# Performance work log

Measured on AMD Instinct MI355X. Metric: run time of the kernel, lower is better.

The kernel has to match this reference:

```python
import jax, jax.numpy as jnp
import numpy as np

PAD = 0.1
RESO = 128           # plane_resolution
HID = 128            # hidden_dim
CDIM = 128           # c_dim
NBLK = 5             # n_blocks
PLANES = (('xz', (0, 2)), ('xy', (0, 1)), ('yz', (1, 2)))


def normalize_coordinate(p, dims):
    # p: (B,T,3) -> (B,T,2) in [0, 1)
    xy = p[..., list(dims)] / (1.0 + PAD + 1e-3) + 0.5
    return jnp.clip(xy, 0.0, 1.0 - 1e-5)


def coordinate2index(xy, reso):
    g = (xy * reso).astype(jnp.int32)          # (B,T,2)
    return g[..., 0] + reso * g[..., 1]        # (B,T) flat cell index


def scatter_max_gather(vals, idx, n_cells):
    # vals: (B,T,F), idx: (B,T) -> per-cell max gathered back to points (B,T,F)
    B, T, F = vals.shape
    flat_idx = (idx + jnp.arange(B, dtype=idx.dtype)[:, None] * n_cells).reshape(-1)
    fea = jax.ops.segment_max(vals.reshape(B * T, F), flat_idx, num_segments=B * n_cells)
    return fea[flat_idx].reshape(B, T, F)


def scatter_mean_plane(c, idx, n_cells):
    # c: (B,T,C), idx: (B,T) -> (B, n_cells, C); empty cells stay 0
    B, T, C = c.shape
    flat_idx = (idx + jnp.arange(B, dtype=idx.dtype)[:, None] * n_cells).reshape(-1)
    s = jax.ops.segment_sum(c.reshape(B * T, C), flat_idx, num_segments=B * n_cells)
    cnt = jax.ops.segment_sum(jnp.ones((B * T,), c.dtype), flat_idx, num_segments=B * n_cells)
    return (s / jnp.maximum(cnt, 1.0)[:, None]).reshape(B, n_cells, C)


def resnet_block(x, W0, b0, W1, b1, Ws):
    # ResnetBlockFC(2H -> H), size_h = H, shortcut = Linear(no bias)
    net = jax.nn.relu(x) @ W0 + b0
    dx = jax.nn.relu(net) @ W1 + b1
    return x @ Ws + dx


def setup_inputs() -> dict:
    key = jax.random.key(0)
    ks = jax.random.split(key, 10)
    B, T = 2, 32768
    s = 0.05
    return {
        'p': jax.random.uniform(ks[0], (B, T, 3), jnp.float32, -0.5, 0.5),
        'fc_pos_W': s * jax.random.normal(ks[1], (3, 2 * HID), jnp.float32),
        'fc_pos_b': s * jax.random.normal(ks[2], (2 * HID,), jnp.float32),
        'blocks_W0': s * jax.random.normal(ks[3], (NBLK, 2 * HID, HID), jnp.float32),
        'blocks_b0': s * jax.random.normal(ks[4], (NBLK, HID), jnp.float32),
        'blocks_W1': s * jax.random.normal(ks[5], (NBLK, HID, HID), jnp.float32),
        'blocks_b1': s * jax.random.normal(ks[6], (NBLK, HID), jnp.float32),
        'blocks_Ws': s * jax.random.normal(ks[7], (NBLK, 2 * HID, HID), jnp.float32),
        'fc_c_W': s * jax.random.normal(ks[8], (HID, CDIM), jnp.float32),
        'fc_c_b': s * jax.random.normal(ks[9], (CDIM,), jnp.float32),
    }


def reference(p, fc_pos_W, fc_pos_b, blocks_W0, blocks_b0, blocks_W1, blocks_b1,
              blocks_Ws, fc_c_W, fc_c_b):
    B, T, _ = p.shape
    R2 = RESO * RESO
    index = {k: coordinate2index(normalize_coordinate(p, d), RESO) for k, d in PLANES}

    net = p @ fc_pos_W + fc_pos_b                       # (B,T,2H)
    net = resnet_block(net, blocks_W0[0], blocks_b0[0],
                       blocks_W1[0], blocks_b1[0], blocks_Ws[0])  # (B,T,H)
    for i in range(1, NBLK):
        pooled = sum(scatter_max_gather(net, index[k], R2) for k, _ in PLANES)
        net = jnp.concatenate([net, pooled], axis=-1)   # (B,T,2H)
        net = resnet_block(net, blocks_W0[i], blocks_b0[i],
                           blocks_W1[i], blocks_b1[i], blocks_Ws[i])

    c = net @ fc_c_W + fc_c_b                           # (B,T,C)
    planes = []
    for k, _ in PLANES:  # order: xz, xy, yz
        fea = scatter_mean_plane(c, index[k], R2)       # (B,R2,C)
        planes.append(fea.transpose(0, 2, 1).reshape(B, CDIM, RESO, RESO))
    return jnp.stack(planes)                            # (3,B,C,R,R)
```

## Files before the change

kernel.cpp:

```cpp
#include <hip/hip_runtime.h>

#define TT 65536
#define R2 16384

typedef _Float16 f16x8 __attribute__((ext_vector_type(8)));
typedef float    f32x4 __attribute__((ext_vector_type(4)));
typedef unsigned u32x4 __attribute__((ext_vector_type(4)));

#define MFMA16 __builtin_amdgcn_mfma_f32_16x16x32_f16

__device__ __forceinline__ unsigned short f2h(float f){
    _Float16 h = (_Float16)f;
    return __builtin_bit_cast(unsigned short, h);
}
__device__ __forceinline__ float h2f(unsigned short u){
    return (float)__builtin_bit_cast(_Float16, u);
}
__device__ __forceinline__ unsigned relu2(unsigned w){
    unsigned s = w & 0x80008000u;
    unsigned mask = ((s >> 15) * 0x7FFFu) | s;
    return w & ~mask;
}
__device__ __forceinline__ float nrm(float a){
    float v = a / 1.101f + 0.5f;
    v = fmaxf(v, 0.0f);
    v = fminf(v, 0.99999f);
    return v;
}

__global__ __launch_bounds__(256) void k_repack(const float* __restrict__ W0,
        const float* __restrict__ W1, const float* __restrict__ Ws,
        const float* __restrict__ Wc, unsigned short* __restrict__ out,
        int* __restrict__ cnt){
    __shared__ unsigned short lh[4096];
    int b = blockIdx.x, tid = threadIdx.x;

    int gid = b*256 + tid;
    if (gid < 24576){ u32x4 z = {0,0,0,0}; ((u32x4*)cnt)[gid] = z; }

    const float* src; int obase;
    if (b < 100){
        int i = b/20, rr = b%20;
        if (rr < 8){       src = W0 + (size_t)i*32768 + rr*4096;      obase = i*81920 + rr*4096; }
        else if (rr < 12){ int ks=rr-8;  src = W1 + (size_t)i*16384 + ks*4096; obase = i*81920 + 32768 + ks*4096; }
        else {             int ks=rr-12; src = Ws + (size_t)i*32768 + ks*4096; obase = i*81920 + 49152 + ks*4096; }
    } else { int ks = b-100; src = Wc + ks*4096; obase = 409600 + ks*4096; }

    #pragma unroll
    for (int m = 0; m < 16; m++){
        int gi = m*256 + tid;
        lh[gi] = f2h(src[gi]);
    }
    __syncthreads();

    #pragma unroll
    for (int g2 = 0; g2 < 2; g2++){
        int base = tid*16 + g2*8;
        int l = (base >> 3) & 63, t = (base >> 9) & 7;
        int n = t*16 + (l & 15), kb = (l >> 4)*8;
        unsigned short h[8];
        #pragma unroll
        for (int j = 0; j < 8; j++) h[j] = lh[(kb + j)*128 + n];
        u32x4 pk;
        #pragma unroll
        for (int q = 0; q < 4; q++)
            pk[q] = (unsigned)h[2*q] | ((unsigned)h[2*q+1] << 16);
        *(u32x4*)(&out[obase + base]) = pk;
    }
}

__global__ __launch_bounds__(256) void k_idxhist(const float* __restrict__ p,
        int* __restrict__ idx, int* __restrict__ cnt){
    int pt = blockIdx.x*256 + threadIdx.x;
    float p0 = p[pt*3+0], p1 = p[pt*3+1], p2 = p[pt*3+2];
    int g0 = (int)(nrm(p0)*128.f);
    int g1 = (int)(nrm(p1)*128.f);
    int g2 = (int)(nrm(p2)*128.f);
    int i0 = g0 + 128*g2, i1 = g0 + 128*g1, i2 = g1 + 128*g2;
    idx[0*TT + pt] = i0;
    idx[1*TT + pt] = i1;
    idx[2*TT + pt] = i2;
    int b14 = (pt >> 15) << 14;
    atomicAdd(&cnt[0*32768 + b14 + i0], 1);
    atomicAdd(&cnt[1*32768 + b14 + i1], 1);
    atomicAdd(&cnt[2*32768 + b14 + i2], 1);
}

__global__ __launch_bounds__(1024) void k_scan(const int* cnt,
        int* __restrict__ cs, int* cp){
    __shared__ int wsum[16];
    int pl = blockIdx.x, tid = threadIdx.x;
    int lane = tid & 63, wid = tid >> 6;
    const int* c = cnt + pl*32768;
    int v[32], tot = 0;
    #pragma unroll
    for (int j = 0; j < 32; j++){ v[j] = c[tid*32 + j]; tot += v[j]; }
    int x = tot;
    #pragma unroll
    for (int off = 1; off < 64; off <<= 1){
        int y = __shfl_up(x, off, 64);
        if (lane >= off) x += y;
    }
    if (lane == 63) wsum[wid] = x;
    __syncthreads();
    int woff = 0;
    #pragma unroll
    for (int j = 0; j < 16; j++) woff += (j < wid) ? wsum[j] : 0;
    int run = woff + x - tot;
    #pragma unroll
    for (int j = 0; j < 32; j++){
        cs[pl*32769 + tid*32 + j] = run;
        cp[pl*32768 + tid*32 + j] = run;
        run += v[j];
    }
    if (tid == 1023) cs[pl*32769 + 32768] = TT;
}

__global__ __launch_bounds__(256) void k_scatter(const int* __restrict__ idx,
        int* __restrict__ cp, int* __restrict__ srt){
    int pt = blockIdx.x*256 + threadIdx.x;
    int b14 = (pt >> 15) << 14;
    #pragma unroll
    for (int pl = 0; pl < 3; pl++){
        int pos = atomicAdd(&cp[pl*32768 + b14 + idx[pl*TT + pt]], 1);
        srt[pl*TT + pos] = pt;
    }
}

__global__ __launch_bounds__(256) void k_pool3(const unsigned short* __restrict__ xb,
        const int* __restrict__ srt, const int* __restrict__ cs,
        unsigned short* __restrict__ mxp){
    int pl = blockIdx.y;
    const int* srtp = srt + (size_t)pl*TT;
    const int* csp  = cs  + (size_t)pl*32769;
    int lane = threadIdx.x & 63, w = threadIdx.x >> 6;
    int g = lane >> 4, l16 = lane & 15;
    int cbase = (blockIdx.x*4 + w)*4;
    for (int c = cbase; c < cbase + 4; c++){
        int s = csp[c], e = csp[c+1];
        if (s == e) continue;
        float fm[8];
        #pragma unroll
        for (int j = 0; j < 8; j++) fm[j] = -1e30f;
        for (int i = s + g; i < e; i += 4){
            int pt = srtp[i];
            u32x4 v = *(const u32x4*)(xb + (size_t)pt*128 + l16*8);
            #pragma unroll
            for (int q = 0; q < 4; q++){
                unsigned u = v[q];
                fm[2*q]   = fmaxf(fm[2*q],   h2f((unsigned short)(u & 0xFFFF)));
                fm[2*q+1] = fmaxf(fm[2*q+1], h2f((unsigned short)(u >> 16)));
            }
        }
        #pragma unroll
        for (int j = 0; j < 8; j++){
            fm[j] = fmaxf(fm[j], __shfl_xor(fm[j], 16, 64));
            fm[j] = fmaxf(fm[j], __shfl_xor(fm[j], 32, 64));
        }
        if (g == 0){
            u32x4 pk;
            #pragma unroll
            for (int q = 0; q < 4; q++)
                pk[q] = (unsigned)f2h(fm[2*q]) | ((unsigned)f2h(fm[2*q+1]) << 16);
            ((u32x4*)(mxp + ((size_t)pl*32768 + c)*128))[l16] = pk;
        }
    }
}

__global__ __launch_bounds__(256, 2) void k_resnet(
        const unsigned short* __restrict__ xin,
        unsigned short* __restrict__ xout,
        const unsigned short* __restrict__ wp,
        const float* __restrict__ b0, const float* __restrict__ b1,
        const int* __restrict__ idx, const unsigned short* __restrict__ mxp,
        const float* __restrict__ pin, const float* __restrict__ fW,
        const float* __restrict__ fb,
        const unsigned short* __restrict__ wc, const float* __restrict__ bc){
    __shared__ __align__(16) unsigned short lds[36864];
    unsigned short* lw0 = lds;
    unsigned short* lw1 = lds + 16384;
    unsigned short* lt  = lds + 32768;
    int tid = threadIdx.x, w = tid >> 6, lane = tid & 63;
    int quad = lane >> 4, l15 = lane & 15;
    int m0 = blockIdx.x*128 + w*32;
    float b0v[8], b1v[8];
    #pragma unroll
    for (int t = 0; t < 8; t++){ b0v[t] = b0[t*16 + l15]; b1v[t] = b1[t*16 + l15]; }

    u32x4 pre[8];
    auto preload = [&](const unsigned short* src){
        const u32x4* g = (const u32x4*)src;
        #pragma unroll
        for (int i = 0; i < 8; i++) pre[i] = g[i*256 + tid];
    };
    auto flushto = [&](unsigned short* dst){
        u32x4* l = (u32x4*)dst;
        #pragma unroll
        for (int i = 0; i < 8; i++) l[i*256 + tid] = pre[i];
    };
    auto gemm = [&](const f16x8* a0, const f16x8* a1, const unsigned short* lwx,
                    f32x4 (&ac)[2][8]){
        #pragma unroll
        for (int ks = 0; ks < 4; ks++){
            #pragma unroll
            for (int t = 0; t < 8; t++){
                f16x8 b = *(const f16x8*)&lwx[((ks*8 + t)*64 + lane)*8];
                ac[0][t] = MFMA16(a0[ks], b, ac[0][t], 0, 0, 0);
                ac[1][t] = MFMA16(a1[ks], b, ac[1][t], 0, 0, 0);
            }
        }
    };

    preload(wp);

    u32x4 xf[2][4]; f16x8 pf[2][4];
    if (pin){
        #pragma unroll
        for (int s = 0; s < 2; s++){
            int row = m0 + s*16 + l15;
            float p0 = pin[row*3+0], p1 = pin[row*3+1], p2 = pin[row*3+2];
            #pragma unroll
            for (int ks = 0; ks < 4; ks++){
                int c0 = ks*32 + quad*8;
                unsigned short hx[8], hp[8];
                #pragma unroll
                for (int h = 0; h < 2; h++){
                    f32x4 w0 = *(const f32x4*)(fW + c0 + h*4);
                    f32x4 w1 = *(const f32x4*)(fW + 256 + c0 + h*4);
                    f32x4 w2 = *(const f32x4*)(fW + 512 + c0 + h*4);
                    f32x4 bb = *(const f32x4*)(fb + c0 + h*4);
                    f32x4 v0 = *(const f32x4*)(fW + 128 + c0 + h*4);
                    f32x4 v1 = *(const f32x4*)(fW + 384 + c0 + h*4);
                    f32x4 v2 = *(const f32x4*)(fW + 640 + c0 + h*4);
                    f32x4 bp = *(const f32x4*)(fb + 128 + c0 + h*4);
                    #pragma unroll
                    for (int j = 0; j < 4; j++){
                        hx[h*4+j] = f2h(bb[j] + p0*w0[j] + p1*w1[j] + p2*w2[j]);
                        hp[h*4+j] = f2h(bp[j] + p0*v0[j] + p1*v1[j] + p2*v2[j]);
                    }
                }
                unsigned short* dx = (unsigned short*)&xf[s][ks];
                unsigned short* dp = (unsigned short*)&pf[s][ks];
                #pragma unroll
                for (int j = 0; j < 8; j++){ dx[j] = hx[j]; dp[j] = hp[j]; }
            }
        }
    } else {
        #pragma unroll
        for (int s = 0; s < 2; s++){
            size_t rb = (size_t)(m0 + s*16 + l15)*128;
            #pragma unroll
            for (int ks = 0; ks < 4; ks++)
                xf[s][ks] = *(const u32x4*)(xin + rb + ks*32 + quad*8);
        }
        #pragma unroll
        for (int s = 0; s < 2; s++){
            int row = m0 + s*16 + l15;
            int b14 = (row >> 15) << 14;
            const unsigned short* q0 = mxp + ((size_t)(0*32768 + b14 + idx[row]))*128;
            const unsigned short* q1 = mxp + ((size_t)(1*32768 + b14 + idx[TT + row]))*128;
            const unsigned short* q2 = mxp + ((size_t)(2*32768 + b14 + idx[2*TT + row]))*128;
            #pragma unroll
            for (int ks = 0; ks < 4; ks++){
                int col = ks*32 + quad*8;
                f16x8 a = *(const f16x8*)(q0 + col);
                f16x8 b = *(const f16x8*)(q1 + col);
                f16x8 c = *(const f16x8*)(q2 + col);
                f16x8 r;
                #pragma unroll
                for (int j = 0; j < 8; j++)
                    r[j] = (_Float16)((float)a[j] + (float)b[j] + (float)c[j]);
                pf[s][ks] = r;
            }
        }
    }

    f16x8 rx[2][4], rp[2][4];
    #pragma unroll
    for (int s = 0; s < 2; s++)
        #pragma unroll
        for (int ks = 0; ks < 4; ks++){
            u32x4 u = xf[s][ks];
            u.x = relu2(u.x); u.y = relu2(u.y); u.z = relu2(u.z); u.w = relu2(u.w);
            rx[s][ks] = __builtin_bit_cast(f16x8, u);
            u32x4 v = __builtin_bit_cast(u32x4, pf[s][ks]);
            v.x = relu2(v.x); v.y = relu2(v.y); v.z = relu2(v.z); v.w = relu2(v.w);
            rp[s][ks] = __builtin_bit_cast(f16x8, v);
        }

    f32x4 acc[2][8];
    #pragma unroll
    for (int s = 0; s < 2; s++)
        #pragma unroll
        for (int t = 0; t < 8; t++){ f32x4 z = {0.f,0.f,0.f,0.f}; acc[s][t] = z; }

    flushto(lw0);
    preload(wp + 16384);
    __syncthreads();

    flushto(lw1);
    preload(wp + 32768);
    gemm(rx[0], rx[1], lw0, acc);
    __syncthreads();

    flushto(lw0);
    preload(wp + 49152);
    gemm(rp[0], rp[1], lw1, acc);
    __syncthreads();

    flushto(lw1);
    preload(wp + 65536);
    f32x4 acc2[2][8];
    #pragma unroll
    for (int s = 0; s < 2; s++)
        #pragma unroll
        for (int t = 0; t < 8; t++){ f32x4 iv = {b1v[t],b1v[t],b1v[t],b1v[t]}; acc2[s][t] = iv; }
    #pragma unroll
    for (int k2 = 0; k2 < 4; k2++){
        if (k2) asm volatile("s_waitcnt lgkmcnt(0)" ::: "memory");
        #pragma unroll
        for (int s = 0; s < 2; s++){
            int strip = w*2 + s;
            #pragma unroll
            for (int tt = 0; tt < 2; tt++){
                int t = k2*2 + tt;
                int l2b = (tt*2 + ((lane >> 3) & 1))*16 + quad*4;
                #pragma unroll
                for (int r = 0; r < 4; r++){
                    float v = fmaxf(acc[s][t][r] + b0v[t], 0.f);
                    lt[((strip*64) + l2b + r)*8 + (lane & 7)] = f2h(v);
                }
            }
        }
        f16x8 a0 = *(const f16x8*)&lt[((w*2 + 0)*64 + lane)*8];
        f16x8 a1 = *(const f16x8*)&lt[((w*2 + 1)*64 + lane)*8];
        #pragma unroll
        for (int t = 0; t < 8; t++){
            f16x8 b = *(const f16x8*)&lw0[((k2*8 + t)*64 + lane)*8];
            acc2[0][t] = MFMA16(a0, b, acc2[0][t], 0, 0, 0);
            acc2[1][t] = MFMA16(a1, b, acc2[1][t], 0, 0, 0);
        }
    }
    __syncthreads();

    flushto(lw0);
    if (wc) preload(wc);
    {
        f16x8 a0[4], a1[4];
        #pragma unroll
        for (int ks = 0; ks < 4; ks++){
            a0[ks] = __builtin_bit_cast(f16x8, xf[0][ks]);
            a1[ks] = __builtin_bit_cast(f16x8, xf[1][ks]);
        }
        gemm(a0, a1, lw1, acc2);
    }
    __syncthreads();

    if (wc) flushto(lw1);
    gemm(pf[0], pf[1], lw0, acc2);

    if (!wc){
        #pragma unroll
        for (int s = 0; s < 2; s++)
            #pragma unroll
            for (int t = 0; t < 8; t++)
                #pragma unroll
                for (int r = 0; r < 4; r++){
                    int row = m0 + s*16 + quad*4 + r;
                    xout[(size_t)row*128 + t*16 + l15] = f2h(acc2[s][t][r]);
                }
        return;
    }
    __syncthreads();

    f32x4 acc3[2][8];
    #pragma unroll
    for (int t = 0; t < 8; t++){
        float bv = bc[t*16 + l15];
        f32x4 iv = {bv, bv, bv, bv};
        acc3[0][t] = iv; acc3[1][t] = iv;
    }
    #pragma unroll
    for (int k2 = 0; k2 < 4; k2++){
        asm volatile("s_waitcnt lgkmcnt(0)" ::: "memory");
        #pragma unroll
        for (int s = 0; s < 2; s++){
            int strip = w*2 + s;
            #pragma unroll
            for (int tt = 0; tt < 2; tt++){
                int t = k2*2 + tt;
                int l2b = (tt*2 + ((lane >> 3) & 1))*16 + quad*4;
                #pragma unroll
                for (int r = 0; r < 4; r++)
                    lt[((strip*64) + l2b + r)*8 + (lane & 7)] = f2h(acc2[s][t][r]);
            }
        }
        f16x8 a0 = *(const f16x8*)&lt[((w*2 + 0)*64 + lane)*8];
        f16x8 a1 = *(const f16x8*)&lt[((w*2 + 1)*64 + lane)*8];
        #pragma unroll
        for (int t = 0; t < 8; t++){
            f16x8 b = *(const f16x8*)&lw1[((k2*8 + t)*64 + lane)*8];
            acc3[0][t] = MFMA16(a0, b, acc3[0][t], 0, 0, 0);
            acc3[1][t] = MFMA16(a1, b, acc3[1][t], 0, 0, 0);
        }
    }
    #pragma unroll
    for (int s = 0; s < 2; s++)
        #pragma unroll
        for (int t = 0; t < 8; t++)
            #pragma unroll
            for (int r = 0; r < 4; r++){
                int row = m0 + s*16 + quad*4 + r;
                xout[(size_t)row*128 + t*16 + l15] = f2h(acc3[s][t][r]);
            }
}

__global__ __launch_bounds__(256) void k_psum3(const unsigned short* __restrict__ cb,
        const int* __restrict__ srt, const int* __restrict__ cs,
        float* __restrict__ out){
    __shared__ float ls[32*129];
    int pl = blockIdx.y;
    const int* srtp = srt + (size_t)pl*TT;
    const int* csp  = cs  + (size_t)pl*32769;
    int tid = threadIdx.x;
    int lane = tid & 63, w = tid >> 6;
    int g = lane >> 4, l16 = lane & 15;
    int c0 = blockIdx.x * 32;
    for (int cc = w*8; cc < w*8 + 8; cc++){
        int c = c0 + cc;
        int s = csp[c], e = csp[c+1];
        float fs[8];
        #pragma unroll
        for (int j = 0; j < 8; j++) fs[j] = 0.f;
        for (int i = s + g; i < e; i += 4){
            int pt = srtp[i];
            u32x4 v = *(const u32x4*)(cb + (size_t)pt*128 + l16*8);
            #pragma unroll
            for (int q = 0; q < 4; q++){
                unsigned u = v[q];
                fs[2*q]   += h2f((unsigned short)(u & 0xFFFF));
                fs[2*q+1] += h2f((unsigned short)(u >> 16));
            }
        }
        #pragma unroll
        for (int j = 0; j < 8; j++){
            fs[j] += __shfl_xor(fs[j], 16, 64);
            fs[j] += __shfl_xor(fs[j], 32, 64);
        }
        float rc = (e > s) ? 1.f/(float)(e - s) : 0.f;
        if (g == 0){
            #pragma unroll
            for (int j = 0; j < 8; j++) ls[cc*129 + l16*8 + j] = fs[j]*rc;
        }
    }
    __syncthreads();
    int pb = pl*2 + (c0 >> 14);
    float* o = out + (size_t)pb*128*R2 + (c0 & 16383);
    #pragma unroll
    for (int k = 0; k < 16; k++){
        int lin = k*256 + tid;
        int f = lin >> 5, cc = lin & 31;
        o[(size_t)f*R2 + cc] = ls[cc*129 + f];
    }
}

extern "C" void kernel_launch(void* const* d_in, const int* in_sizes, int n_in,
                              void* d_out, int out_size, void* d_ws, size_t ws_size,
                              hipStream_t stream) {
    const float* p        = (const float*)d_in[0];
    const float* fc_pos_W = (const float*)d_in[1];
    const float* fc_pos_b = (const float*)d_in[2];
    const float* bW0      = (const float*)d_in[3];
    const float* bb0      = (const float*)d_in[4];
    const float* bW1      = (const float*)d_in[5];
    const float* bb1      = (const float*)d_in[6];
    const float* bWs      = (const float*)d_in[7];
    const float* fc_c_W   = (const float*)d_in[8];
    const float* fc_c_b   = (const float*)d_in[9];
    float* out = (float*)d_out;

    char* ws = (char*)d_ws;
    int*            idx   = (int*)ws;
    unsigned short* net0  = (unsigned short*)(ws + 786432);
    unsigned short* net1  = (unsigned short*)(ws + 17563648);
    unsigned short* cbuf  = (unsigned short*)(ws + 34340864);
    int*            srt   = (int*)(ws + 51118080);
    int*            cs    = (int*)(ws + 51904512);
    int*            cp    = (int*)(ws + 52297744);
    unsigned short* wpack = (unsigned short*)(ws + 52690960);
    unsigned short* mxp   = (unsigned short*)(ws + 53542928);

    const unsigned short* NUS = (const unsigned short*)nullptr;
    const float* NF = (const float*)nullptr;

    k_repack <<<104, 256, 0, stream>>>(bW0, bW1, bWs, fc_c_W, wpack, cp);
    k_idxhist<<<256, 256, 0, stream>>>(p, idx, cp);
    k_scan   <<<3, 1024, 0, stream>>>(cp, cs, cp);
    k_scatter<<<256, 256, 0, stream>>>(idx, cp, srt);

    k_resnet<<<512, 256, 0, stream>>>(NUS, net0, wpack, bb0, bb1,
            idx, NUS, p, fc_pos_W, fc_pos_b, NUS, NF);

    k_pool3<<<dim3(2048, 3), 256, 0, stream>>>(net0, srt, cs, mxp);
    k_resnet<<<512, 256, 0, stream>>>(net0, net1, wpack + 81920,
            bb0 + 128, bb1 + 128, idx, mxp, NF, NF, NF, NUS, NF);
    k_pool3<<<dim3(2048, 3), 256, 0, stream>>>(net1, srt, cs, mxp);
    k_resnet<<<512, 256, 0, stream>>>(net1, net0, wpack + 163840,
            bb0 + 256, bb1 + 256, idx, mxp, NF, NF, NF, NUS, NF);
    k_pool3<<<dim3(2048, 3), 256, 0, stream>>>(net0, srt, cs, mxp);
    k_resnet<<<512, 256, 0, stream>>>(net0, net1, wpack + 245760,
            bb0 + 384, bb1 + 384, idx, mxp, NF, NF, NF, NUS, NF);
    k_pool3<<<dim3(2048, 3), 256, 0, stream>>>(net1, srt, cs, mxp);
    k_resnet<<<512, 256, 0, stream>>>(net1, cbuf, wpack + 327680,
            bb0 + 512, bb1 + 512, idx, mxp, NF, NF, NF,
            wpack + 409600, fc_c_b);

    k_psum3<<<dim3(1024, 3), 256, 0, stream>>>(cbuf, srt, cs, out);
}
```

Before: 389.2 us.

## Read ResNet weight fragments directly from global memory instead of staging in LDS

Removes the double-buffered LDS staging of weight tiles and the block-wide barriers around it. Each MFMA B-fragment is now loaded straight from global memory, relying on L1/L2 caching since every block reads the same weights. LDS shrinks to the small transpose buffer, and launch bounds are raised to 3 blocks per CU to gain occupancy. The cost is that each wave issues its own global weight loads, with higher latency and no shared reuse through LDS.

```diff
diff --git a/kernel.cpp b/kernel.cpp
--- a/kernel.cpp
+++ b/kernel.cpp
@@ -167,7 +167,7 @@
     }
 }
 
-__global__ __launch_bounds__(256, 2) void k_resnet(
+__global__ __launch_bounds__(256, 3) void k_resnet(
         const unsigned short* __restrict__ xin,
         unsigned short* __restrict__ xout,
         const unsigned short* __restrict__ wp,
@@ -176,10 +176,7 @@
         const float* __restrict__ pin, const float* __restrict__ fW,
         const float* __restrict__ fb,
         const unsigned short* __restrict__ wc, const float* __restrict__ bc){
-    __shared__ __align__(16) unsigned short lds[36864];
-    unsigned short* lw0 = lds;
-    unsigned short* lw1 = lds + 16384;
-    unsigned short* lt  = lds + 32768;
+    __shared__ __align__(16) unsigned short lt[4096];
     int tid = threadIdx.x, w = tid >> 6, lane = tid & 63;
     int quad = lane >> 4, l15 = lane & 15;
     int m0 = blockIdx.x*128 + w*32;
@@ -187,31 +184,18 @@
     #pragma unroll
     for (int t = 0; t < 8; t++){ b0v[t] = b0[t*16 + l15]; b1v[t] = b1[t*16 + l15]; }
 
-    u32x4 pre[8];
-    auto preload = [&](const unsigned short* src){
-        const u32x4* g = (const u32x4*)src;
-        #pragma unroll
-        for (int i = 0; i < 8; i++) pre[i] = g[i*256 + tid];
-    };
-    auto flushto = [&](unsigned short* dst){
-        u32x4* l = (u32x4*)dst;
-        #pragma unroll
-        for (int i = 0; i < 8; i++) l[i*256 + tid] = pre[i];
-    };
-    auto gemm = [&](const f16x8* a0, const f16x8* a1, const unsigned short* lwx,
+    auto gemm = [&](const f16x8* a0, const f16x8* a1, const unsigned short* wg,
                     f32x4 (&ac)[2][8]){
         #pragma unroll
         for (int ks = 0; ks < 4; ks++){
             #pragma unroll
             for (int t = 0; t < 8; t++){
-                f16x8 b = *(const f16x8*)&lwx[((ks*8 + t)*64 + lane)*8];
+                f16x8 b = *(const f16x8*)&wg[((ks*8 + t)*64 + lane)*8];
                 ac[0][t] = MFMA16(a0[ks], b, ac[0][t], 0, 0, 0);
                 ac[1][t] = MFMA16(a1[ks], b, ac[1][t], 0, 0, 0);
             }
         }
     };
-
-    preload(wp);
 
     u32x4 xf[2][4]; f16x8 pf[2][4];
     if (pin){
@@ -275,46 +259,45 @@
         }
     }
 
-    f16x8 rx[2][4], rp[2][4];
+    f32x4 acc[2][8];
     #pragma unroll
     for (int s = 0; s < 2; s++)
         #pragma unroll
+        for (int t = 0; t < 8; t++){ f32x4 z = {0.f,0.f,0.f,0.f}; acc[s][t] = z; }
+
+    {
+        f16x8 a0[4], a1[4];
+        #pragma unroll
         for (int ks = 0; ks < 4; ks++){
-            u32x4 u = xf[s][ks];
-            u.x = relu2(u.x); u.y = relu2(u.y); u.z = relu2(u.z); u.w = relu2(u.w);
-            rx[s][ks] = __builtin_bit_cast(f16x8, u);
-            u32x4 v = __builtin_bit_cast(u32x4, pf[s][ks]);
-            v.x = relu2(v.x); v.y = relu2(v.y); v.z = relu2(v.z); v.w = relu2(v.w);
-            rp[s][ks] = __builtin_bit_cast(f16x8, v);
-        }
-
-    f32x4 acc[2][8];
+            u32x4 u0 = xf[0][ks], u1 = xf[1][ks];
+            u0.x = relu2(u0.x); u0.y = relu2(u0.y); u0.z = relu2(u0.z); u0.w = relu2(u0.w);
+            u1.x = relu2(u1.x); u1.y = relu2(u1.y); u1.z = relu2(u1.z); u1.w = relu2(u1.w);
+            a0[ks] = __builtin_bit_cast(f16x8, u0);
+            a1[ks] = __builtin_bit_cast(f16x8, u1);
+        }
+        gemm(a0, a1, wp, acc);
+    }
+
+    {
+        f16x8 a0[4], a1[4];
+        #pragma unroll
+        for (int ks = 0; ks < 4; ks++){
+            u32x4 u0 = __builtin_bit_cast(u32x4, pf[0][ks]);
+            u32x4 u1 = __builtin_bit_cast(u32x4, pf[1][ks]);
+            u0.x = relu2(u0.x); u0.y = relu2(u0.y); u0.z = relu2(u0.z); u0.w = relu2(u0.w);
+            u1.x = relu2(u1.x); u1.y = relu2(u1.y); u1.z = relu2(u1.z); u1.w = relu2(u1.w);
+            a0[ks] = __builtin_bit_cast(f16x8, u0);
+            a1[ks] = __builtin_bit_cast(f16x8, u1);
+        }
+        gemm(a0, a1, wp + 16384, acc);
+    }
+
+    f32x4 acc2[2][8];
     #pragma unroll
     for (int s = 0; s < 2; s++)
         #pragma unroll
-        for (int t = 0; t < 8; t++){ f32x4 z = {0.f,0.f,0.f,0.f}; acc[s][t] = z; }
-
-    flushto(lw0);
-    preload(wp + 16384);
-    __syncthreads();
-
-    flushto(lw1);
-    preload(wp + 32768);
-    gemm(rx[0], rx[1], lw0, acc);
-    __syncthreads();
-
-    flushto(lw0);
-    preload(wp + 49152);
-    gemm(rp[0], rp[1], lw1, acc);
-    __syncthreads();
-
-    flushto(lw1);
-    preload(wp + 65536);
-    f32x4 acc2[2][8];
-    #pragma unroll
-    for (int s = 0; s < 2; s++)
-        #pragma unroll
         for (int t = 0; t < 8; t++){ f32x4 iv = {b1v[t],b1v[t],b1v[t],b1v[t]}; acc2[s][t] = iv; }
+    const unsigned short* w1g = wp + 32768;
     #pragma unroll
     for (int k2 = 0; k2 < 4; k2++){
         if (k2) asm volatile("s_waitcnt lgkmcnt(0)" ::: "memory");
@@ -336,15 +319,12 @@
         f16x8 a1 = *(const f16x8*)&lt[((w*2 + 1)*64 + lane)*8];
         #pragma unroll
         for (int t = 0; t < 8; t++){
-            f16x8 b = *(const f16x8*)&lw0[((k2*8 + t)*64 + lane)*8];
+            f16x8 b = *(const f16x8*)&w1g[((k2*8 + t)*64 + lane)*8];
             acc2[0][t] = MFMA16(a0, b, acc2[0][t], 0, 0, 0);
             acc2[1][t] = MFMA16(a1, b, acc2[1][t], 0, 0, 0);
         }
     }
-    __syncthreads();
-
-    flushto(lw0);
-    if (wc) preload(wc);
+
     {
         f16x8 a0[4], a1[4];
         #pragma unroll
@@ -352,12 +332,10 @@
             a0[ks] = __builtin_bit_cast(f16x8, xf[0][ks]);
             a1[ks] = __builtin_bit_cast(f16x8, xf[1][ks]);
         }
-        gemm(a0, a1, lw1, acc2);
-    }
-    __syncthreads();
-
-    if (wc) flushto(lw1);
-    gemm(pf[0], pf[1], lw0, acc2);
+        gemm(a0, a1, wp + 49152, acc2);
+    }
+
+    gemm(pf[0], pf[1], wp + 65536, acc2);
 
     if (!wc){
         #pragma unroll
@@ -371,7 +349,6 @@
                 }
         return;
     }
-    __syncthreads();
 
     f32x4 acc3[2][8];
     #pragma unroll
@@ -399,7 +376,7 @@
         f16x8 a1 = *(const f16x8*)&lt[((w*2 + 1)*64 + lane)*8];
         #pragma unroll
         for (int t = 0; t < 8; t++){
-            f16x8 b = *(const f16x8*)&lw1[((k2*8 + t)*64 + lane)*8];
+            f16x8 b = *(const f16x8*)&wc[((k2*8 + t)*64 + lane)*8];
             acc3[0][t] = MFMA16(a0, b, acc3[0][t], 0, 0, 0);
             acc3[1][t] = MFMA16(a1, b, acc3[1][t], 0, 0, 0);
         }
```

Result: slower. 599.7 us (+54.1%).
